# Optimization experiments

Measured on AMD Instinct MI355X. Metric: run time of the kernel, lower is better.

The kernel has to match this reference:

```python
import jax, jax.numpy as jnp
import numpy as np


def _conv(x, w, b=None, stride=1, pad=0, groups=1):
    y = jax.lax.conv_general_dilated(x, w, (stride, stride), [(pad, pad), (pad, pad)],
                                     feature_group_count=groups,
                                     dimension_numbers=('NCHW', 'OIHW', 'NCHW'))
    return y if b is None else y + b[None, :, None, None]


def _ln_c(x, g, b, eps=1e-5):
    # LayerNorm2d: normalize over channel axis of NCHW
    mu = x.mean(axis=1, keepdims=True)
    var = ((x - mu) ** 2).mean(axis=1, keepdims=True)
    return (x - mu) * jax.lax.rsqrt(var + eps) * g[None, :, None, None] + b[None, :, None, None]


def _ln_last(x, g, b, eps=1e-5):
    mu = x.mean(-1, keepdims=True)
    var = ((x - mu) ** 2).mean(-1, keepdims=True)
    return (x - mu) * jax.lax.rsqrt(var + eps) * g + b


def _resize(x, hw):
    B, C, _, _ = x.shape
    return jax.image.resize(x, (B, C, hw[0], hw[1]), method='bilinear')


def _ss2d(x, in_w, cv_w, cv_b, xp_w, dtp_w, dtp_b, Alog, Dsk, on_g, on_b, out_w):
    # x: (B,H,W,C) channels-last; VMamba SS2D v2 (cross-scan selective scan)
    B, H, W, C = x.shape
    D = in_w.shape[0] // 2
    K, Ck, _ = xp_w.shape
    R = dtp_w.shape[-1]
    N = (Ck - R) // 2
    L = H * W
    xz = x @ in_w.T                                   # (B,H,W,2D)
    xc, z = jnp.split(xz, 2, axis=-1)
    xc = jax.nn.silu(_conv(jnp.transpose(xc, (0, 3, 1, 2)), cv_w, cv_b, pad=1, groups=D))
    x0 = xc.reshape(B, D, L)
    x1 = jnp.transpose(xc, (0, 1, 3, 2)).reshape(B, D, L)
    xs = jnp.stack([x0, x1, jnp.flip(x0, -1), jnp.flip(x1, -1)], axis=1)  # (B,K,D,L)
    x_dbl = jnp.einsum('bkdl,kcd->bkcl', xs, xp_w)
    dts, Bs, Cs = jnp.split(x_dbl, [R, R + N], axis=2)
    dt = jax.nn.softplus(jnp.einsum('bkrl,kdr->bkdl', dts, dtp_w) + dtp_b[None, :, :, None])
    A = -jnp.exp(Alog).reshape(K, D, N)
    a = jnp.exp(dt[..., None] * A[None, :, :, None, :])                  # (B,K,D,L,N)
    bmat = (dt * xs)[..., None] * jnp.transpose(Bs, (0, 1, 3, 2))[:, :, None, :, :]

    def comb(e1, e2):
        a1, b1 = e1
        a2, b2 = e2
        return a1 * a2, a2 * b1 + b2

    _, h = jax.lax.associative_scan(comb, (a, bmat), axis=3)             # h: (B,K,D,L,N)
    y = jnp.einsum('bkdln,bknl->bkdl', h, Cs) + Dsk.reshape(K, D)[None, :, :, None] * xs

    def inv_t(t):
        return jnp.transpose(t.reshape(B, D, W, H), (0, 1, 3, 2)).reshape(B, D, L)

    ym = y[:, 0] + inv_t(y[:, 1]) + jnp.flip(y[:, 2], -1) + inv_t(jnp.flip(y[:, 3], -1))
    ym = _ln_last(jnp.transpose(ym.reshape(B, D, H, W), (0, 2, 3, 1)), on_g, on_b)
    return (ym * jax.nn.silu(z)) @ out_w.T


def _mcfa(x, shortcut, q_w, q_b, sr_w, sr_b, srn_g, srn_b, k_w, k_b, v_w, v_b, mp_w, mp_b,
          key_dim=16, sr=2):
    # cross attention: queries from x, keys/values from spatially-reduced shortcut
    B, C, H, W = x.shape
    heads = C // key_dim
    q = _conv(x, q_w, q_b).reshape(B, heads, key_dim, H * W)
    s = _ln_c(_conv(shortcut, sr_w, sr_b, stride=sr), srn_g, srn_b)
    Lk = s.shape[2] * s.shape[3]
    k = _conv(s, k_w, k_b).reshape(B, heads, key_dim, Lk)
    v = _conv(s, v_w, v_b).reshape(B, heads, C // heads, Lk)
    scale = float(key_dim) ** 0.5
    attn = jax.nn.softmax(jnp.einsum('bhdq,bhdk->bhqk', q, k) / scale, axis=-1)
    o = jnp.einsum('bhqk,bhdk->bhdq', attn, v).reshape(B, C, H, W)
    return _conv(o, mp_w, mp_b)


def _forward(x, res, shortcut_mfkm, rc0_w, rcp_w, rcp_g, rcp_b, pe_w, pe_b,
             n1_g, n1_b, n2_g, n2_b, q_w, q_b, sr_w, sr_b, srn_g, srn_b,
             k_w, k_b, v_w, v_b, mp_w, mp_b, in_w, cv_w, cv_b, xp_w, dtp_w, dtp_b,
             Alog, Dsk, on_g, on_b, out_w, ls1_w, ls1_b, ls2_w, ls2_b,
             f1_w, f1_b, f2_w, f2_b):
    # Res_conv
    pad1 = res.mean(axis=1, keepdims=True)
    pad2 = res.max(axis=1, keepdims=True)
    r = jnp.concatenate([_conv(res, rc0_w), pad1, pad2], axis=1)          # (B,66,H,W)
    B, Ct, H, W = r.shape
    r = jnp.transpose(r.reshape(B, Ct // 3, 3, H, W), (0, 2, 1, 3, 4)).reshape(B, Ct, H, W)
    r = _conv(r, rcp_w, pad=1)
    bn_scale = rcp_g * jax.lax.rsqrt(jnp.float32(1.0 + 1e-5))             # eval BN, mean=0 var=1
    r = jnp.clip(r * bn_scale[None, :, None, None] + rcp_b[None, :, None, None], 0.0, 6.0)
    sm = _resize(shortcut_mfkm, (H, W))
    shortcut = jnp.concatenate([r, sm], axis=1)                           # 130 channels
    inp = _resize(x, (2 * x.shape[2], 2 * x.shape[3]))
    # _forward of the block (is_first=True, is_last=False, eval: dropout/droppath identity)
    t = inp + _conv(inp, pe_w, pe_b, pad=1, groups=inp.shape[1])
    m = _mcfa(_ln_c(t, n1_g, n1_b), shortcut, q_w, q_b, sr_w, sr_b, srn_g, srn_b,
              k_w, k_b, v_w, v_b, mp_w, mp_b)
    m = jnp.transpose(_ss2d(jnp.transpose(m, (0, 2, 3, 1)), in_w, cv_w, cv_b, xp_w,
                            dtp_w, dtp_b, Alog, Dsk, on_g, on_b, out_w), (0, 3, 1, 2))
    t = t * ls1_w[None, :, None, None] + ls1_b[None, :, None, None] + m   # layerscale_1 + residual
    u = _conv(_ln_c(t, n2_g, n2_b), f1_w, f1_b)
    u = _conv(jax.nn.gelu(u, approximate=False), f2_w, f2_b)
    t = t * ls2_w[None, :, None, None] + ls2_b[None, :, None, None] + u   # layerscale_2 + mlp
    return t


def setup_inputs():
    key = jax.random.key(0)
    ks = iter(jax.random.split(key, 64))

    def rn(shape, s=0.02):
        return jax.random.normal(next(ks), shape, dtype=jnp.float32) * s

    B, C, Hin, Win, RC, CD, Ct, Din, K, N, R, MH = 2, 64, 32, 32, 32, 130, 66, 128, 4, 16, 4, 256
    return {
        'x': rn((B, C, Hin, Win), 1.0),
        'res': rn((B, RC, 2 * Hin, 2 * Win), 1.0),
        'shortcut_mfkm': rn((B, C, Hin, Win), 1.0),
        'rc0_w': rn((C, RC, 1, 1)),
        'rcp_w': rn((Ct, Ct, 3, 3)),
        'rcp_g': jnp.ones((Ct,), jnp.float32),
        'rcp_b': jnp.zeros((Ct,), jnp.float32),
        'pe_w': rn((C, 1, 3, 3)),
        'pe_b': jnp.zeros((C,), jnp.float32),
        'n1_g': jnp.ones((C,), jnp.float32),
        'n1_b': jnp.zeros((C,), jnp.float32),
        'n2_g': jnp.ones((C,), jnp.float32),
        'n2_b': jnp.zeros((C,), jnp.float32),
        'q_w': rn((C, C, 1, 1)),
        'q_b': jnp.zeros((C,), jnp.float32),
        'sr_w': rn((CD, CD, 2, 2)),
        'sr_b': jnp.zeros((CD,), jnp.float32),
        'srn_g': jnp.ones((CD,), jnp.float32),
        'srn_b': jnp.zeros((CD,), jnp.float32),
        'k_w': rn((C, CD, 1, 1)),
        'k_b': jnp.zeros((C,), jnp.float32),
        'v_w': rn((C, CD, 1, 1)),
        'v_b': jnp.zeros((C,), jnp.float32),
        'mp_w': rn((C, C, 1, 1)),
        'mp_b': jnp.zeros((C,), jnp.float32),
        'in_w': rn((2 * Din, C)),
        'cv_w': rn((Din, 1, 3, 3)),
        'cv_b': jnp.zeros((Din,), jnp.float32),
        'xp_w': rn((K, R + 2 * N, Din)),
        'dtp_w': rn((K, Din, R), 0.1),
        'dtp_b': rn((K, Din), 0.1),
        'Alog': jnp.log(jnp.tile(jnp.arange(1, N + 1, dtype=jnp.float32), (K * Din, 1))),
        'Dsk': jnp.ones((K * Din,), jnp.float32),
        'on_g': jnp.ones((Din,), jnp.float32),
        'on_b': jnp.zeros((Din,), jnp.float32),
        'out_w': rn((C, Din)),
        'ls1_w': jnp.full((C,), 1e-5, jnp.float32),
        'ls1_b': jnp.zeros((C,), jnp.float32),
        'ls2_w': jnp.full((C,), 1e-5, jnp.float32),
        'ls2_b': jnp.zeros((C,), jnp.float32),
        'f1_w': rn((MH, C, 1, 1)),
        'f1_b': jnp.zeros((MH,), jnp.float32),
        'f2_w': rn((C, MH, 1, 1)),
        'f2_b': jnp.zeros((C,), jnp.float32),
    }


def reference(x, res, shortcut_mfkm, rc0_w, rcp_w, rcp_g, rcp_b, pe_w, pe_b,
              n1_g, n1_b, n2_g, n2_b, q_w, q_b, sr_w, sr_b, srn_g, srn_b,
              k_w, k_b, v_w, v_b, mp_w, mp_b, in_w, cv_w, cv_b, xp_w, dtp_w, dtp_b,
              Alog, Dsk, on_g, on_b, out_w, ls1_w, ls1_b, ls2_w, ls2_b,
              f1_w, f1_b, f2_w, f2_b):
    t = _forward(x, res, shortcut_mfkm, rc0_w, rcp_w, rcp_g, rcp_b, pe_w, pe_b,
                 n1_g, n1_b, n2_g, n2_b, q_w, q_b, sr_w, sr_b, srn_g, srn_b,
                 k_w, k_b, v_w, v_b, mp_w, mp_b, in_w, cv_w, cv_b, xp_w, dtp_w, dtp_b,
                 Alog, Dsk, on_g, on_b, out_w, ls1_w, ls1_b, ls2_w, ls2_b,
                 f1_w, f1_b, f2_w, f2_b)
    return (t, t)  # (x, shortcut) with shortcut == x in the non-last branch
```

## Files before the change

### kernel.cpp

```cpp
#include <hip/hip_runtime.h>
#include <math.h>

#define B2 2
#define HW 4096
#define L4 4096
#define NCH 16
#define CLEN 256

enum : size_t {
  OFF_INP    = 0,
  OFF_SHORT  = 524288,
  OFF_RSHUF  = 1589248,
  OFF_XLN    = 2129920,
  OFF_SRAW   = 2654208,
  OFF_SRED   = 2920448,
  OFF_QT     = 3186688,
  OFF_KT     = 3710976,
  OFF_VT     = 3842048,
  OFF_OT     = 3973120,
  OFF_M0     = 4497408,
  OFF_XC     = 3186688,
  OFF_U1     = 0,
  OFF_T      = 5021696,
  OFF_T1     = 5545984,
  OFF_Z      = 6070272,
  OFF_XC2    = 7118848,
  OFF_XC2T   = 8167424,
  OFF_PROJ   = 9216000,
  OFF_APROD  = 10395648,
  OFF_HEND   = 10657792,
  OFF_SSTART = 10919936,
  OFF_YM     = 11182080,
  OFF_PART   = 7118848,
};

__global__ void k_rconv0(const float* __restrict__ res, const float* __restrict__ rc0_w,
                         float* __restrict__ rshuf) {
  int idx = blockIdx.x * 256 + threadIdx.x;
  if (idx >= B2 * 66 * HW) return;
  int p = idx & (HW - 1);
  int bc = idx >> 12;
  int c = bc % 66, b = bc / 66;
  int cc = (c % 22) * 3 + (c / 22);
  const float* rb = res + (size_t)b * 32 * HW + p;
  float v;
  if (cc < 64) {
    const float* w = rc0_w + cc * 32;
    float a = 0.f;
#pragma unroll
    for (int ic = 0; ic < 32; ++ic) a = fmaf(w[ic], rb[ic * HW], a);
    v = a;
  } else if (cc == 64) {
    float s = 0.f;
#pragma unroll
    for (int ic = 0; ic < 32; ++ic) s += rb[ic * HW];
    v = s * (1.f / 32.f);
  } else {
    float m = rb[0];
#pragma unroll
    for (int ic = 1; ic < 32; ++ic) m = fmaxf(m, rb[ic * HW]);
    v = m;
  }
  rshuf[idx] = v;
}

__global__ __launch_bounds__(256) void k_rconv3(const float* __restrict__ rshuf,
                                                const float* __restrict__ rcp_w,
                                                const float* __restrict__ rcp_g,
                                                const float* __restrict__ rcp_b,
                                                float* __restrict__ shortcut) {
  __shared__ float lw[6 * 594];
  int cg = blockIdx.y % 11, b = blockIdx.y / 11;
  int c0 = cg * 6;
  for (int i = threadIdx.x; i < 6 * 594; i += 256) lw[i] = rcp_w[c0 * 594 + i];
  __syncthreads();
  int p = blockIdx.x * 256 + threadIdx.x;
  int h = p >> 6, w = p & 63;
  float acc[6] = {0, 0, 0, 0, 0, 0};
  for (int ci = 0; ci < 66; ++ci) {
    const float* ib = rshuf + (size_t)(b * 66 + ci) * HW;
#pragma unroll
    for (int kh = -1; kh <= 1; ++kh) {
      int hh = h + kh;
      if (hh < 0 || hh > 63) continue;
#pragma unroll
      for (int kw = -1; kw <= 1; ++kw) {
        int ww = w + kw;
        if (ww < 0 || ww > 63) continue;
        float x = ib[hh * 64 + ww];
        int tap = ci * 9 + (kh + 1) * 3 + (kw + 1);
#pragma unroll
        for (int u = 0; u < 6; ++u) acc[u] = fmaf(lw[u * 594 + tap], x, acc[u]);
      }
    }
  }
  const float bscale = rsqrtf(1.f + 1e-5f);
#pragma unroll
  for (int u = 0; u < 6; ++u) {
    int co = c0 + u;
    float v = acc[u] * (rcp_g[co] * bscale) + rcp_b[co];
    v = fminf(fmaxf(v, 0.f), 6.f);
    shortcut[(size_t)(b * 130 + co) * HW + p] = v;
  }
}

__global__ void k_up(const float* __restrict__ smf, const float* __restrict__ x,
                     float* __restrict__ shortcut, float* __restrict__ inp) {
  int idx = blockIdx.x * 256 + threadIdx.x;
  if (idx >= B2 * 128 * HW) return;
  int p = idx & (HW - 1);
  int bc = idx >> 12;
  int c = bc & 127, b = bc >> 7;
  int oh = p >> 6, ow = p & 63;
  int hp = oh >> 1, wp = ow >> 1;
  int ih0, ih1, iw0, iw1;
  float wh0, ww0;
  if (oh & 1) { ih0 = hp; ih1 = (hp + 1 > 31) ? 31 : hp + 1; wh0 = 0.75f; }
  else        { ih0 = (hp - 1 < 0) ? 0 : hp - 1; ih1 = hp; wh0 = 0.25f; }
  if (ow & 1) { iw0 = wp; iw1 = (wp + 1 > 31) ? 31 : wp + 1; ww0 = 0.75f; }
  else        { iw0 = (wp - 1 < 0) ? 0 : wp - 1; iw1 = wp; ww0 = 0.25f; }
  const float* src = (c < 64) ? (smf + (size_t)(b * 64 + c) * 1024)
                              : (x + (size_t)(b * 64 + (c - 64)) * 1024);
  float v00 = src[ih0 * 32 + iw0], v01 = src[ih0 * 32 + iw1];
  float v10 = src[ih1 * 32 + iw0], v11 = src[ih1 * 32 + iw1];
  float v = wh0 * (ww0 * v00 + (1.f - ww0) * v01) + (1.f - wh0) * (ww0 * v10 + (1.f - ww0) * v11);
  if (c < 64) shortcut[(size_t)(b * 130 + 66 + c) * HW + p] = v;
  else        inp[(size_t)(b * 64 + (c - 64)) * HW + p] = v;
}

__global__ void k_pe(const float* __restrict__ inp, const float* __restrict__ pe_w,
                     const float* __restrict__ pe_b, float* __restrict__ t) {
  int idx = blockIdx.x * 256 + threadIdx.x;
  if (idx >= B2 * 64 * HW) return;
  int p = idx & (HW - 1);
  int bc = idx >> 12;
  int c = bc & 63;
  int h = p >> 6, w = p & 63;
  const float* ib = inp + (size_t)bc * HW;
  const float* wt = pe_w + c * 9;
  float a = pe_b[c];
#pragma unroll
  for (int kh = -1; kh <= 1; ++kh) {
    int hh = h + kh;
    if (hh < 0 || hh > 63) continue;
#pragma unroll
    for (int kw = -1; kw <= 1; ++kw) {
      int ww = w + kw;
      if (ww < 0 || ww > 63) continue;
      a = fmaf(wt[(kh + 1) * 3 + (kw + 1)], ib[hh * 64 + ww], a);
    }
  }
  t[idx] = ib[p] + a;
}

__global__ void k_lnc64(const float* __restrict__ in, const float* __restrict__ g,
                        const float* __restrict__ bb, float* __restrict__ out) {
  int idx = blockIdx.x * 256 + threadIdx.x;
  if (idx >= B2 * HW) return;
  int p = idx & (HW - 1), b = idx >> 12;
  const float* ib = in + (size_t)b * 64 * HW + p;
  float s = 0.f, sq = 0.f;
#pragma unroll 8
  for (int c = 0; c < 64; ++c) { float v = ib[c * HW]; s += v; sq = fmaf(v, v, sq); }
  float mu = s * (1.f / 64.f);
  float var = sq * (1.f / 64.f) - mu * mu;
  float rs = rsqrtf(var + 1e-5f);
  float* ob = out + (size_t)b * 64 * HW + p;
#pragma unroll 8
  for (int c = 0; c < 64; ++c) ob[c * HW] = (ib[c * HW] - mu) * rs * g[c] + bb[c];
}

__global__ __launch_bounds__(256) void k_sr(const float* __restrict__ shortcut,
                                            const float* __restrict__ sr_w,
                                            const float* __restrict__ sr_b,
                                            float* __restrict__ sraw) {
  __shared__ float lw[5 * 520];
  int cg = blockIdx.y % 26, b = blockIdx.y / 26;
  int c0 = cg * 5;
  for (int i = threadIdx.x; i < 5 * 520; i += 256) lw[i] = sr_w[c0 * 520 + i];
  __syncthreads();
  int op = blockIdx.x * 256 + threadIdx.x;
  int oh = op >> 5, ow = op & 31;
  const float* ib = shortcut + (size_t)b * 130 * HW + (oh * 2) * 64 + ow * 2;
  float acc[5] = {0, 0, 0, 0, 0};
  for (int ci = 0; ci < 130; ++ci) {
    const float* q = ib + (size_t)ci * HW;
    float x00 = q[0], x01 = q[1], x10 = q[64], x11 = q[65];
#pragma unroll
    for (int u = 0; u < 5; ++u) {
      const float* wp = lw + u * 520 + ci * 4;
      acc[u] = fmaf(wp[0], x00, fmaf(wp[1], x01, fmaf(wp[2], x10, fmaf(wp[3], x11, acc[u]))));
    }
  }
#pragma unroll
  for (int u = 0; u < 5; ++u)
    sraw[(size_t)(b * 130 + c0 + u) * 1024 + op] = acc[u] + sr_b[c0 + u];
}

__global__ __launch_bounds__(64) void k_ln130(const float* __restrict__ sraw,
                                              const float* __restrict__ g,
                                              const float* __restrict__ bb,
                                              float* __restrict__ sred) {
  int op = blockIdx.x & 1023, b = blockIdx.x >> 10;
  int t = threadIdx.x;
  const float* ib = sraw + (size_t)b * 130 * 1024 + op;
  float s = 0.f, sq = 0.f;
  for (int c = t; c < 130; c += 64) { float v = ib[c * 1024]; s += v; sq = fmaf(v, v, sq); }
#pragma unroll
  for (int off = 32; off; off >>= 1) { s += __shfl_xor(s, off); sq += __shfl_xor(sq, off); }
  float mu = s * (1.f / 130.f);
  float var = sq * (1.f / 130.f) - mu * mu;
  float rs = rsqrtf(var + 1e-5f);
  float* ob = sred + (size_t)b * 130 * 1024 + op;
  for (int c = t; c < 130; c += 64) ob[c * 1024] = (ib[c * 1024] - mu) * rs * g[c] + bb[c];
}

__global__ void k_kv(const float* __restrict__ sred, const float* __restrict__ k_w,
                     const float* __restrict__ k_b, const float* __restrict__ v_w,
                     const float* __restrict__ v_b, float* __restrict__ kt, float* __restrict__ vt) {
  int idx = blockIdx.x * 256 + threadIdx.x;
  if (idx >= B2 * 128 * 1024) return;
  int op = idx & 1023;
  int bc = idx >> 10;
  int c = bc & 127, b = bc >> 7;
  bool isv = c >= 64;
  int co = c & 63;
  const float* w = (isv ? v_w : k_w) + co * 130;
  const float* ib = sred + (size_t)b * 130 * 1024 + op;
  float a = (isv ? v_b : k_b)[co];
  for (int ci = 0; ci < 130; ++ci) a = fmaf(w[ci], ib[ci * 1024], a);
  float* dst = isv ? vt : kt;
  dst[((size_t)(b * 4 + (co >> 4)) * 1024 + op) * 16 + (co & 15)] = a;
}

__global__ void k_q(const float* __restrict__ xln, const float* __restrict__ q_w,
                    const float* __restrict__ q_b, float* __restrict__ qt) {
  int idx = blockIdx.x * 256 + threadIdx.x;
  if (idx >= B2 * 64 * HW) return;
  int p = idx & (HW - 1);
  int bc = idx >> 12;
  int co = bc & 63, b = bc >> 6;
  const float* ib = xln + (size_t)b * 64 * HW + p;
  const float* w = q_w + co * 64;
  float a = q_b[co];
#pragma unroll
  for (int ci = 0; ci < 64; ++ci) a = fmaf(w[ci], ib[ci * HW], a);
  qt[((size_t)(b * 4 + (co >> 4)) * HW + p) * 16 + (co & 15)] = a;
}

__global__ __launch_bounds__(256) void k_attn1(const float* __restrict__ qt,
                                               const float* __restrict__ kt,
                                               const float* __restrict__ vt,
                                               float* __restrict__ part) {
  __shared__ float sk[256 * 16];
  __shared__ float sv[256 * 16];
  int ktile = blockIdx.x, qtile = blockIdx.y, bh = blockIdx.z;
  int tid = threadIdx.x;
  const float* kb = kt + ((size_t)bh * 1024 + ktile * 256) * 16;
  const float* vb = vt + ((size_t)bh * 1024 + ktile * 256) * 16;
  for (int i = tid * 4; i < 4096; i += 1024) {
    *(float4*)&sk[i] = *(const float4*)&kb[i];
    *(float4*)&sv[i] = *(const float4*)&vb[i];
  }
  __syncthreads();
  int q = qtile * 256 + tid;
  const float4* qr = (const float4*)(qt + ((size_t)bh * HW + q) * 16);
  float4 q0 = qr[0], q1 = qr[1], q2 = qr[2], q3 = qr[3];
  const float sc = 0.25f;
  q0.x *= sc; q0.y *= sc; q0.z *= sc; q0.w *= sc;
  q1.x *= sc; q1.y *= sc; q1.z *= sc; q1.w *= sc;
  q2.x *= sc; q2.y *= sc; q2.z *= sc; q2.w *= sc;
  q3.x *= sc; q3.y *= sc; q3.z *= sc; q3.w *= sc;
  float m = -1e30f, l = 0.f;
  float acc[16];
#pragma unroll
  for (int i = 0; i < 16; ++i) acc[i] = 0.f;
  for (int kk = 0; kk < 256; ++kk) {
    const float4* kr = (const float4*)&sk[kk * 16];
    float4 a0 = kr[0], a1 = kr[1], a2 = kr[2], a3 = kr[3];
    float s = q0.x * a0.x + q0.y * a0.y + q0.z * a0.z + q0.w * a0.w
            + q1.x * a1.x + q1.y * a1.y + q1.z * a1.z + q1.w * a1.w
            + q2.x * a2.x + q2.y * a2.y + q2.z * a2.z + q2.w * a2.w
            + q3.x * a3.x + q3.y * a3.y + q3.z * a3.z + q3.w * a3.w;
    if (s > m) {
      float r = __expf(m - s);
      l *= r;
#pragma unroll
      for (int i = 0; i < 16; ++i) acc[i] *= r;
      m = s;
    }
    float pe = __expf(s - m);
    l += pe;
    const float4* vr = (const float4*)&sv[kk * 16];
    float4 b0 = vr[0], b1 = vr[1], b2 = vr[2], b3 = vr[3];
    acc[0] = fmaf(pe, b0.x, acc[0]);  acc[1] = fmaf(pe, b0.y, acc[1]);
    acc[2] = fmaf(pe, b0.z, acc[2]);  acc[3] = fmaf(pe, b0.w, acc[3]);
    acc[4] = fmaf(pe, b1.x, acc[4]);  acc[5] = fmaf(pe, b1.y, acc[5]);
    acc[6] = fmaf(pe, b1.z, acc[6]);  acc[7] = fmaf(pe, b1.w, acc[7]);
    acc[8] = fmaf(pe, b2.x, acc[8]);  acc[9] = fmaf(pe, b2.y, acc[9]);
    acc[10] = fmaf(pe, b2.z, acc[10]); acc[11] = fmaf(pe, b2.w, acc[11]);
    acc[12] = fmaf(pe, b3.x, acc[12]); acc[13] = fmaf(pe, b3.y, acc[13]);
    acc[14] = fmaf(pe, b3.z, acc[14]); acc[15] = fmaf(pe, b3.w, acc[15]);
  }
  float* o = part + (((size_t)bh * 4 + ktile) * HW + q) * 18;
#pragma unroll
  for (int i = 0; i < 16; ++i) o[i] = acc[i];
  o[16] = m;
  o[17] = l;
}

__global__ void k_attn2(const float* __restrict__ part, float* __restrict__ ot) {
  int idx = blockIdx.x * 256 + threadIdx.x;
  if (idx >= B2 * 4 * HW) return;
  int q = idx & (HW - 1), bh = idx >> 12;
  float M = -1e30f;
#pragma unroll
  for (int kt4 = 0; kt4 < 4; ++kt4)
    M = fmaxf(M, part[(((size_t)bh * 4 + kt4) * HW + q) * 18 + 16]);
  float L = 0.f;
  float o[16];
#pragma unroll
  for (int i = 0; i < 16; ++i) o[i] = 0.f;
#pragma unroll
  for (int kt4 = 0; kt4 < 4; ++kt4) {
    const float* p = part + (((size_t)bh * 4 + kt4) * HW + q) * 18;
    float w = __expf(p[16] - M);
    L = fmaf(p[17], w, L);
#pragma unroll
    for (int i = 0; i < 16; ++i) o[i] = fmaf(p[i], w, o[i]);
  }
  float inv = 1.f / L;
  float* ob = ot + ((size_t)bh * HW + q) * 16;
#pragma unroll
  for (int i = 0; i < 16; ++i) ob[i] = o[i] * inv;
}

__global__ void k_mp(const float* __restrict__ ot, const float* __restrict__ mp_w,
                     const float* __restrict__ mp_b, float* __restrict__ m0) {
  int idx = blockIdx.x * 256 + threadIdx.x;
  if (idx >= B2 * 64 * HW) return;
  int p = idx & (HW - 1);
  int bc = idx >> 12;
  int co = bc & 63, b = bc >> 6;
  const float* w = mp_w + co * 64;
  float a = mp_b[co];
#pragma unroll
  for (int h = 0; h < 4; ++h) {
    const float* ob = ot + ((size_t)(b * 4 + h) * HW + p) * 16;
#pragma unroll
    for (int d = 0; d < 16; ++d) a = fmaf(w[h * 16 + d], ob[d], a);
  }
  m0[idx] = a;
}

__global__ __launch_bounds__(256) void k_inproj(const float* __restrict__ m0,
                                                const float* __restrict__ in_w,
                                                float* __restrict__ xc, float* __restrict__ z) {
  __shared__ float lw[4 * 64];
  int jg = blockIdx.y & 63, b = blockIdx.y >> 6;
  int j0 = jg * 4;
  for (int i = threadIdx.x; i < 256; i += 256) lw[i] = in_w[j0 * 64 + i];
  __syncthreads();
  int p = blockIdx.x * 256 + threadIdx.x;
  const float* ib = m0 + (size_t)b * 64 * HW + p;
  float acc[4] = {0, 0, 0, 0};
#pragma unroll 8
  for (int ci = 0; ci < 64; ++ci) {
    float x = ib[ci * HW];
#pragma unroll
    for (int u = 0; u < 4; ++u) acc[u] = fmaf(lw[u * 64 + ci], x, acc[u]);
  }
#pragma unroll
  for (int u = 0; u < 4; ++u) {
    int j = j0 + u;
    if (j < 128) xc[(size_t)(b * 128 + j) * HW + p] = acc[u];
    else         z[(size_t)(b * 128 + j - 128) * HW + p] = acc[u];
  }
}

__global__ void k_dw(const float* __restrict__ xc, const float* __restrict__ cv_w,
                     const float* __restrict__ cv_b, float* __restrict__ xc2) {
  int idx = blockIdx.x * 256 + threadIdx.x;
  if (idx >= B2 * 128 * HW) return;
  int p = idx & (HW - 1);
  int bc = idx >> 12;
  int c = bc & 127;
  int h = p >> 6, w = p & 63;
  const float* ib = xc + (size_t)bc * HW;
  const float* wt = cv_w + c * 9;
  float a = cv_b[c];
#pragma unroll
  for (int kh = -1; kh <= 1; ++kh) {
    int hh = h + kh;
    if (hh < 0 || hh > 63) continue;
#pragma unroll
    for (int kw = -1; kw <= 1; ++kw) {
      int ww = w + kw;
      if (ww < 0 || ww > 63) continue;
      a = fmaf(wt[(kh + 1) * 3 + (kw + 1)], ib[hh * 64 + ww], a);
    }
  }
  xc2[idx] = a / (1.f + __expf(-a));
}

__global__ void k_tr(const float* __restrict__ xc2, float* __restrict__ xc2t) {
  int idx = blockIdx.x * 256 + threadIdx.x;
  if (idx >= B2 * 128 * HW) return;
  int l = idx & (HW - 1);
  size_t bd = (size_t)(idx >> 12);
  xc2t[idx] = xc2[(bd << 12) + ((l & 63) << 6) + (l >> 6)];
}

__global__ __launch_bounds__(256) void k_projs(const float* __restrict__ xc2,
                                               const float* __restrict__ xc2t,
                                               const float* __restrict__ xp_w,
                                               float* __restrict__ proj) {
  __shared__ float lw[6 * 128];
  int cg = blockIdx.y % 6;
  int bk = blockIdx.y / 6;
  int b = bk >> 2, k = bk & 3;
  int c0 = cg * 6;
  for (int i = threadIdx.x; i < 768; i += 256) lw[i] = xp_w[(k * 36 + c0) * 128 + i];
  __syncthreads();
  int l = blockIdx.x * 256 + threadIdx.x;
  const float* src = ((k & 1) ? xc2t : xc2) + (size_t)b * 128 * HW;
  int lx = (k >= 2) ? (4095 - l) : l;
  float acc[6] = {0, 0, 0, 0, 0, 0};
#pragma unroll 4
  for (int d = 0; d < 128; ++d) {
    float x = src[(size_t)d * HW + lx];
#pragma unroll
    for (int u = 0; u < 6; ++u) acc[u] = fmaf(lw[u * 128 + d], x, acc[u]);
  }
#pragma unroll
  for (int u = 0; u < 6; ++u)
    proj[(size_t)(bk * 36 + c0 + u) * L4 + l] = acc[u];
}

template <int PC>
__global__ __launch_bounds__(256) void k_scan(const float* __restrict__ proj,
                                              const float* __restrict__ xc2,
                                              const float* __restrict__ xc2t,
                                              const float* __restrict__ dtp_w,
                                              const float* __restrict__ dtp_b,
                                              const float* __restrict__ Alog,
                                              const float* __restrict__ Dsk,
                                              float* __restrict__ aprod,
                                              float* __restrict__ hend,
                                              const float* __restrict__ sstart,
                                              float* __restrict__ ympre) {
  int ch = blockIdx.x, dg = blockIdx.y, bk = blockIdx.z;
  int b = bk >> 2, k = bk & 3;
  int tid = threadIdx.x;
  int n = tid & 15, dl = tid >> 4;
  int d = dg * 16 + dl;
  int kd = k * 128 + d;
  float Ad = -__expf(Alog[kd * 16 + n]);
  const float* wr = dtp_w + kd * 4;
  float w0 = wr[0], w1 = wr[1], w2 = wr[2], w3 = wr[3];
  float db = dtp_b[kd];
  const float* pb = proj + (size_t)bk * 36 * L4;
  const float* srcb = ((k & 1) ? xc2t : xc2) + (size_t)b * 128 * HW;
  bool rev = (k >= 2);
  float h = PC ? sstart[((size_t)(bk * 128 + d) * 16 + n) * NCH + ch] : 0.f;
  float ap = 1.f;
  float Dv = PC ? Dsk[kd] : 0.f;
  __shared__ float sdts[4][16];
  __shared__ float sB[16][17];
  __shared__ float sC[16][17];
  __shared__ float sx[16][16];
  __shared__ float sdt[16][16];
  int l0 = ch * CLEN;
  for (int t0 = 0; t0 < CLEN; t0 += 16) {
    int lb = l0 + t0;
    __syncthreads();
    if (tid < 64) sdts[tid >> 4][tid & 15] = pb[(size_t)(tid >> 4) * L4 + lb + (tid & 15)];
    sB[dl][n] = pb[(size_t)(4 + dl) * L4 + lb + n];
    if (PC) sC[dl][n] = pb[(size_t)(20 + dl) * L4 + lb + n];
    {
      int l = lb + n;
      int lx = rev ? (4095 - l) : l;
      sx[dl][n] = srcb[(size_t)(dg * 16 + dl) * HW + lx];
    }
    __syncthreads();
    {
      float xr = fmaf(w0, sdts[0][n], fmaf(w1, sdts[1][n], fmaf(w2, sdts[2][n], fmaf(w3, sdts[3][n], db))));
      float spv = (xr > 20.f) ? xr : log1pf(__expf(xr));
      sdt[dl][n] = spv;
    }
    __syncthreads();
#pragma unroll 4
    for (int t = 0; t < 16; ++t) {
      float dt = sdt[dl][t];
      float xs = sx[dl][t];
      float a = __expf(dt * Ad);
      h = fmaf(a, h, dt * xs * sB[n][t]);
      if (PC) {
        float yv = h * sC[n][t];
        yv += __shfl_xor(yv, 1);
        yv += __shfl_xor(yv, 2);
        yv += __shfl_xor(yv, 4);
        yv += __shfl_xor(yv, 8);
        if (n == 0) {
          int l = lb + t;
          int pp;
          if (k == 0) pp = l;
          else if (k == 1) pp = ((l & 63) << 6) | (l >> 6);
          else if (k == 2) pp = 4095 - l;
          else { int lf = 4095 - l; pp = ((lf & 63) << 6) | (lf >> 6); }
          atomicAdd(ympre + ((size_t)b * HW + pp) * 128 + d, yv + Dv * xs);
        }
      } else {
        ap *= a;
      }
    }
  }
  if (!PC) {
    size_t o = ((size_t)(bk * 128 + d) * 16 + n) * NCH + ch;
    aprod[o] = ap;
    hend[o] = h;
  }
}

__global__ void k_scanB(const float* __restrict__ aprod, const float* __restrict__ hend,
                        float* __restrict__ sstart) {
  int idx = blockIdx.x * 256 + threadIdx.x;
  if (idx >= B2 * 4 * 128 * 16) return;
  const float* ap = aprod + (size_t)idx * NCH;
  const float* he = hend + (size_t)idx * NCH;
  float* ss = sstart + (size_t)idx * NCH;
  float s = 0.f;
#pragma unroll
  for (int c = 0; c < NCH; ++c) { ss[c] = s; s = fmaf(ap[c], s, he[c]); }
}

__global__ __launch_bounds__(128) void k_merge(const float* __restrict__ ympre,
                                               const float* __restrict__ z,
                                               const float* __restrict__ on_g,
                                               const float* __restrict__ on_b,
                                               float* __restrict__ g) {
  int p = blockIdx.x & (HW - 1), b = blockIdx.x >> 12;
  int d = threadIdx.x;
  float v = ympre[((size_t)b * HW + p) * 128 + d];
  float s = v, sq = v * v;
#pragma unroll
  for (int off = 32; off; off >>= 1) { s += __shfl_xor(s, off); sq += __shfl_xor(sq, off); }
  __shared__ float sh[4];
  if ((threadIdx.x & 63) == 0) { sh[(threadIdx.x >> 6) * 2] = s; sh[(threadIdx.x >> 6) * 2 + 1] = sq; }
  __syncthreads();
  float S = sh[0] + sh[2], SQ = sh[1] + sh[3];
  float mu = S * (1.f / 128.f);
  float var = SQ * (1.f / 128.f) - mu * mu;
  float rs = rsqrtf(var + 1e-5f);
  float gn = (v - mu) * rs * on_g[d] + on_b[d];
  float zv = z[((size_t)(b * 128 + d)) * HW + p];
  float sil = zv / (1.f + __expf(-zv));
  g[((size_t)b * HW + p) * 128 + d] = gn * sil;
}

__global__ __launch_bounds__(256) void k_outproj(const float* __restrict__ g,
                                                 const float* __restrict__ out_w,
                                                 const float* __restrict__ t,
                                                 const float* __restrict__ ls1_w,
                                                 const float* __restrict__ ls1_b,
                                                 float* __restrict__ t1) {
  __shared__ float lw[4 * 128];
  int cg = blockIdx.y & 15, b = blockIdx.y >> 4;
  int c0 = cg * 4;
  for (int i = threadIdx.x; i < 512; i += 256) lw[i] = out_w[c0 * 128 + i];
  __syncthreads();
  int p = blockIdx.x * 256 + threadIdx.x;
  const float* gr = g + ((size_t)b * HW + p) * 128;
  float acc[4] = {0, 0, 0, 0};
#pragma unroll 4
  for (int dd = 0; dd < 128; ++dd) {
    float x = gr[dd];
#pragma unroll
    for (int u = 0; u < 4; ++u) acc[u] = fmaf(lw[u * 128 + dd], x, acc[u]);
  }
#pragma unroll
  for (int u = 0; u < 4; ++u) {
    int co = c0 + u;
    size_t o = (size_t)(b * 64 + co) * HW + p;
    t1[o] = fmaf(t[o], ls1_w[co], ls1_b[co]) + acc[u];
  }
}

__global__ __launch_bounds__(256) void k_f1(const float* __restrict__ xln2,
                                            const float* __restrict__ f1_w,
                                            const float* __restrict__ f1_b,
                                            float* __restrict__ u1) {
  __shared__ float lw[8 * 64];
  int cg = blockIdx.y & 31, b = blockIdx.y >> 5;
  int c0 = cg * 8;
  for (int i = threadIdx.x; i < 512; i += 256) lw[i] = f1_w[c0 * 64 + i];
  __syncthreads();
  int p = blockIdx.x * 256 + threadIdx.x;
  const float* ib = xln2 + (size_t)b * 64 * HW + p;
  float acc[8] = {0, 0, 0, 0, 0, 0, 0, 0};
#pragma unroll 8
  for (int ci = 0; ci < 64; ++ci) {
    float x = ib[ci * HW];
#pragma unroll
    for (int u = 0; u < 8; ++u) acc[u] = fmaf(lw[u * 64 + ci], x, acc[u]);
  }
#pragma unroll
  for (int u = 0; u < 8; ++u) {
    float v = acc[u] + f1_b[c0 + u];
    v = 0.5f * v * (1.f + erff(v * 0.70710678118654752440f));
    u1[(size_t)(b * 256 + c0 + u) * HW + p] = v;
  }
}

__global__ __launch_bounds__(256) void k_f2(const float* __restrict__ u1,
                                            const float* __restrict__ f2_w,
                                            const float* __restrict__ f2_b,
                                            const float* __restrict__ t1,
                                            const float* __restrict__ ls2_w,
                                            const float* __restrict__ ls2_b,
                                            float* __restrict__ out) {
  __shared__ float lw[4 * 256];
  int cg = blockIdx.y & 15, b = blockIdx.y >> 4;
  int c0 = cg * 4;
  for (int i = threadIdx.x; i < 1024; i += 256) lw[i] = f2_w[c0 * 256 + i];
  __syncthreads();
  int p = blockIdx.x * 256 + threadIdx.x;
  const float* ib = u1 + (size_t)b * 256 * HW + p;
  float acc[4] = {0, 0, 0, 0};
#pragma unroll 4
  for (int ci = 0; ci < 256; ++ci) {
    float x = ib[(size_t)ci * HW];
#pragma unroll
    for (int u = 0; u < 4; ++u) acc[u] = fmaf(lw[u * 256 + ci], x, acc[u]);
  }
#pragma unroll
  for (int u = 0; u < 4; ++u) {
    int co = c0 + u;
    size_t o = (size_t)(b * 64 + co) * HW + p;
    float v = fmaf(t1[o], ls2_w[co], ls2_b[co]) + acc[u] + f2_b[co];
    out[o] = v;
    out[o + (size_t)B2 * 64 * HW] = v;
  }
}

extern "C" void kernel_launch(void* const* d_in, const int* in_sizes, int n_in,
                              void* d_out, int out_size, void* d_ws, size_t ws_size,
                              hipStream_t stream) {
  const float* x     = (const float*)d_in[0];
  const float* res   = (const float*)d_in[1];
  const float* smf   = (const float*)d_in[2];
  const float* rc0_w = (const float*)d_in[3];
  const float* rcp_w = (const float*)d_in[4];
  const float* rcp_g = (const float*)d_in[5];
  const float* rcp_b = (const float*)d_in[6];
  const float* pe_w  = (const float*)d_in[7];
  const float* pe_b  = (const float*)d_in[8];
  const float* n1_g  = (const float*)d_in[9];
  const float* n1_b  = (const float*)d_in[10];
  const float* n2_g  = (const float*)d_in[11];
  const float* n2_b  = (const float*)d_in[12];
  const float* q_w   = (const float*)d_in[13];
  const float* q_b   = (const float*)d_in[14];
  const float* sr_w  = (const float*)d_in[15];
  const float* sr_b  = (const float*)d_in[16];
  const float* srn_g = (const float*)d_in[17];
  const float* srn_b = (const float*)d_in[18];
  const float* k_w   = (const float*)d_in[19];
  const float* k_b   = (const float*)d_in[20];
  const float* v_w   = (const float*)d_in[21];
  const float* v_b   = (const float*)d_in[22];
  const float* mp_w  = (const float*)d_in[23];
  const float* mp_b  = (const float*)d_in[24];
  const float* in_w  = (const float*)d_in[25];
  const float* cv_w  = (const float*)d_in[26];
  const float* cv_b  = (const float*)d_in[27];
  const float* xp_w  = (const float*)d_in[28];
  const float* dtp_w = (const float*)d_in[29];
  const float* dtp_b = (const float*)d_in[30];
  const float* Alog  = (const float*)d_in[31];
  const float* Dsk   = (const float*)d_in[32];
  const float* on_g  = (const float*)d_in[33];
  const float* on_b  = (const float*)d_in[34];
  const float* out_w = (const float*)d_in[35];
  const float* ls1_w = (const float*)d_in[36];
  const float* ls1_b = (const float*)d_in[37];
  const float* ls2_w = (const float*)d_in[38];
  const float* ls2_b = (const float*)d_in[39];
  const float* f1_w  = (const float*)d_in[40];
  const float* f1_b  = (const float*)d_in[41];
  const float* f2_w  = (const float*)d_in[42];
  const float* f2_b  = (const float*)d_in[43];
  float* ws = (float*)d_ws;
  float* out = (float*)d_out;

  k_rconv0<<<dim3(2112), dim3(256), 0, stream>>>(res, rc0_w, ws + OFF_RSHUF);
  k_rconv3<<<dim3(16, 22), dim3(256), 0, stream>>>(ws + OFF_RSHUF, rcp_w, rcp_g, rcp_b, ws + OFF_SHORT);
  k_up<<<dim3(4096), dim3(256), 0, stream>>>(smf, x, ws + OFF_SHORT, ws + OFF_INP);
  k_pe<<<dim3(2048), dim3(256), 0, stream>>>(ws + OFF_INP, pe_w, pe_b, ws + OFF_T);
  k_lnc64<<<dim3(32), dim3(256), 0, stream>>>(ws + OFF_T, n1_g, n1_b, ws + OFF_XLN);
  k_sr<<<dim3(4, 52), dim3(256), 0, stream>>>(ws + OFF_SHORT, sr_w, sr_b, ws + OFF_SRAW);
  k_ln130<<<dim3(2048), dim3(64), 0, stream>>>(ws + OFF_SRAW, srn_g, srn_b, ws + OFF_SRED);
  k_kv<<<dim3(1024), dim3(256), 0, stream>>>(ws + OFF_SRED, k_w, k_b, v_w, v_b, ws + OFF_KT, ws + OFF_VT);
  k_q<<<dim3(2048), dim3(256), 0, stream>>>(ws + OFF_XLN, q_w, q_b, ws + OFF_QT);
  k_attn1<<<dim3(4, 16, 8), dim3(256), 0, stream>>>(ws + OFF_QT, ws + OFF_KT, ws + OFF_VT, ws + OFF_PART);
  k_attn2<<<dim3(128), dim3(256), 0, stream>>>(ws + OFF_PART, ws + OFF_OT);
  k_mp<<<dim3(2048), dim3(256), 0, stream>>>(ws + OFF_OT, mp_w, mp_b, ws + OFF_M0);
  k_inproj<<<dim3(16, 128), dim3(256), 0, stream>>>(ws + OFF_M0, in_w, ws + OFF_XC, ws + OFF_Z);
  k_dw<<<dim3(4096), dim3(256), 0, stream>>>(ws + OFF_XC, cv_w, cv_b, ws + OFF_XC2);
  k_tr<<<dim3(4096), dim3(256), 0, stream>>>(ws + OFF_XC2, ws + OFF_XC2T);
  k_projs<<<dim3(16, 48), dim3(256), 0, stream>>>(ws + OFF_XC2, ws + OFF_XC2T, xp_w, ws + OFF_PROJ);
  k_scan<0><<<dim3(NCH, 8, 8), dim3(256), 0, stream>>>(ws + OFF_PROJ, ws + OFF_XC2, ws + OFF_XC2T,
      dtp_w, dtp_b, Alog, Dsk, ws + OFF_APROD, ws + OFF_HEND, ws + OFF_SSTART, ws + OFF_YM);
  k_scanB<<<dim3(64), dim3(256), 0, stream>>>(ws + OFF_APROD, ws + OFF_HEND, ws + OFF_SSTART);
  hipMemsetAsync(ws + OFF_YM, 0, (size_t)B2 * HW * 128 * sizeof(float), stream);
  k_scan<1><<<dim3(NCH, 8, 8), dim3(256), 0, stream>>>(ws + OFF_PROJ, ws + OFF_XC2, ws + OFF_XC2T,
      dtp_w, dtp_b, Alog, Dsk, ws + OFF_APROD, ws + OFF_HEND, ws + OFF_SSTART, ws + OFF_YM);
  k_merge<<<dim3(8192), dim3(128), 0, stream>>>(ws + OFF_YM, ws + OFF_Z, on_g, on_b, ws + OFF_YM);
  k_outproj<<<dim3(16, 32), dim3(256), 0, stream>>>(ws + OFF_YM, out_w, ws + OFF_T, ls1_w, ls1_b, ws + OFF_T1);
  k_lnc64<<<dim3(32), dim3(256), 0, stream>>>(ws + OFF_T1, n2_g, n2_b, ws + OFF_XLN);
  k_f1<<<dim3(16, 64), dim3(256), 0, stream>>>(ws + OFF_XLN, f1_w, f1_b, ws + OFF_U1);
  k_f2<<<dim3(16, 32), dim3(256), 0, stream>>>(ws + OFF_U1, f2_w, f2_b, ws + OFF_T1, ls2_w, ls2_b, out);
}
```

Before: 621.0 us.

## Restructure selective scan: one thread per channel holding all 16 states, 64 chunks

The chunked selective scan now gives each thread one channel d and keeps all 16 state entries in registers, instead of one thread per (d,n) with shuffle reductions. The sequence is split into 64 chunks of 64 rather than 16 of 256. The chunk decay product is computed as exp(A*sum(dt)) instead of a running product, and chunk state buffers move to a chunk-major layout in reused workspace. This aims to remove per-step warp shuffles, to load dt/B/C/x once per block, and to shorten the serial path per chunk, at the cost of more registers and a longer cross-chunk pass in scanB.

```diff
diff --git a/kernel.cpp b/kernel.cpp
--- a/kernel.cpp
+++ b/kernel.cpp
@@ -4,10 +4,12 @@
 #define B2 2
 #define HW 4096
 #define L4 4096
-#define NCH 16
-#define CLEN 256
+#define NCH 64
 
 enum : size_t {
+  OFF_APROD  = 0,
+  OFF_HEND   = 1048576,
+  OFF_SSTART = 2097152,
   OFF_INP    = 0,
   OFF_SHORT  = 524288,
   OFF_RSHUF  = 1589248,
@@ -27,9 +29,6 @@
   OFF_XC2    = 7118848,
   OFF_XC2T   = 8167424,
   OFF_PROJ   = 9216000,
-  OFF_APROD  = 10395648,
-  OFF_HEND   = 10657792,
-  OFF_SSTART = 10919936,
   OFF_YM     = 11182080,
   OFF_PART   = 7118848,
 };
@@ -438,100 +437,147 @@
 }
 
 template <int PC>
-__global__ __launch_bounds__(256) void k_scan(const float* __restrict__ proj,
-                                              const float* __restrict__ xc2,
-                                              const float* __restrict__ xc2t,
-                                              const float* __restrict__ dtp_w,
-                                              const float* __restrict__ dtp_b,
-                                              const float* __restrict__ Alog,
-                                              const float* __restrict__ Dsk,
-                                              float* __restrict__ aprod,
-                                              float* __restrict__ hend,
-                                              const float* __restrict__ sstart,
-                                              float* __restrict__ ympre) {
-  int ch = blockIdx.x, dg = blockIdx.y, bk = blockIdx.z;
+__global__ __launch_bounds__(256) void k_scan2(const float* __restrict__ proj,
+                                               const float* __restrict__ xc2,
+                                               const float* __restrict__ xc2t,
+                                               const float* __restrict__ dtp_w,
+                                               const float* __restrict__ dtp_b,
+                                               const float* __restrict__ Alog,
+                                               const float* __restrict__ Dsk,
+                                               float* __restrict__ aprod,
+                                               float* __restrict__ hend,
+                                               const float* __restrict__ sstart,
+                                               float* __restrict__ ympre) {
+  __shared__ float sxs[2][128][33];
+  __shared__ float sB[2][16][32];
+  __shared__ float sC[2][16][32];
+  __shared__ float sdts[2][4][32];
+  int tid = threadIdx.x;
+  int hid = tid >> 7;
+  int dl = tid & 127;
+  int ch = blockIdx.x * 2 + hid;
+  int bk = blockIdx.y;
   int b = bk >> 2, k = bk & 3;
-  int tid = threadIdx.x;
-  int n = tid & 15, dl = tid >> 4;
-  int d = dg * 16 + dl;
+  int d = dl;
   int kd = k * 128 + d;
-  float Ad = -__expf(Alog[kd * 16 + n]);
-  const float* wr = dtp_w + kd * 4;
-  float w0 = wr[0], w1 = wr[1], w2 = wr[2], w3 = wr[3];
+  float Ad[16];
+  {
+    const float4* a4 = (const float4*)(Alog + (size_t)kd * 16);
+#pragma unroll
+    for (int i = 0; i < 4; ++i) {
+      float4 v = a4[i];
+      Ad[i * 4 + 0] = -__expf(v.x); Ad[i * 4 + 1] = -__expf(v.y);
+      Ad[i * 4 + 2] = -__expf(v.z); Ad[i * 4 + 3] = -__expf(v.w);
+    }
+  }
+  float4 wv = *(const float4*)(dtp_w + (size_t)kd * 4);
   float db = dtp_b[kd];
+  float Dv = PC ? Dsk[kd] : 0.f;
+  float h[16];
+  if (PC) {
+    const float4* s4 = (const float4*)(sstart + (size_t)ch * 16384 + (size_t)(bk * 128 + d) * 16);
+#pragma unroll
+    for (int i = 0; i < 4; ++i) {
+      float4 v = s4[i];
+      h[i * 4 + 0] = v.x; h[i * 4 + 1] = v.y; h[i * 4 + 2] = v.z; h[i * 4 + 3] = v.w;
+    }
+  } else {
+#pragma unroll
+    for (int i = 0; i < 16; ++i) h[i] = 0.f;
+  }
+  float ssum = 0.f;
   const float* pb = proj + (size_t)bk * 36 * L4;
   const float* srcb = ((k & 1) ? xc2t : xc2) + (size_t)b * 128 * HW;
   bool rev = (k >= 2);
-  float h = PC ? sstart[((size_t)(bk * 128 + d) * 16 + n) * NCH + ch] : 0.f;
-  float ap = 1.f;
-  float Dv = PC ? Dsk[kd] : 0.f;
-  __shared__ float sdts[4][16];
-  __shared__ float sB[16][17];
-  __shared__ float sC[16][17];
-  __shared__ float sx[16][16];
-  __shared__ float sdt[16][16];
-  int l0 = ch * CLEN;
-  for (int t0 = 0; t0 < CLEN; t0 += 16) {
-    int lb = l0 + t0;
+
+  for (int tile = 0; tile < 2; ++tile) {
+    int lb = ch * 64 + tile * 32;
     __syncthreads();
-    if (tid < 64) sdts[tid >> 4][tid & 15] = pb[(size_t)(tid >> 4) * L4 + lb + (tid & 15)];
-    sB[dl][n] = pb[(size_t)(4 + dl) * L4 + lb + n];
-    if (PC) sC[dl][n] = pb[(size_t)(20 + dl) * L4 + lb + n];
-    {
-      int l = lb + n;
+#pragma unroll
+    for (int i = 0; i < 9; ++i) {
+      int flat = i * 128 + dl;
+      int row = flat >> 5, col = flat & 31;
+      float v = pb[(size_t)row * L4 + lb + col];
+      if (row < 4) sdts[hid][row][col] = v;
+      else if (row < 20) sB[hid][row - 4][col] = v;
+      else sC[hid][row - 20][col] = v;
+    }
+#pragma unroll
+    for (int i = 0; i < 32; ++i) {
+      int flat = i * 128 + dl;
+      int dd = flat >> 5, t = flat & 31;
+      int l = lb + t;
       int lx = rev ? (4095 - l) : l;
-      sx[dl][n] = srcb[(size_t)(dg * 16 + dl) * HW + lx];
+      sxs[hid][dd][t] = srcb[(size_t)dd * HW + lx];
     }
     __syncthreads();
-    {
-      float xr = fmaf(w0, sdts[0][n], fmaf(w1, sdts[1][n], fmaf(w2, sdts[2][n], fmaf(w3, sdts[3][n], db))));
-      float spv = (xr > 20.f) ? xr : log1pf(__expf(xr));
-      sdt[dl][n] = spv;
-    }
-    __syncthreads();
-#pragma unroll 4
-    for (int t = 0; t < 16; ++t) {
-      float dt = sdt[dl][t];
-      float xs = sx[dl][t];
-      float a = __expf(dt * Ad);
-      h = fmaf(a, h, dt * xs * sB[n][t]);
+#pragma unroll
+    for (int tg = 0; tg < 32; tg += 4) {
+      float spv[4], xsv[4], dxs[4];
+#pragma unroll
+      for (int j = 0; j < 4; ++j) {
+        int t = tg + j;
+        float dtr = fmaf(wv.x, sdts[hid][0][t], fmaf(wv.y, sdts[hid][1][t],
+                    fmaf(wv.z, sdts[hid][2][t], fmaf(wv.w, sdts[hid][3][t], db))));
+        float sp = (dtr > 20.f) ? dtr : log1pf(__expf(dtr));
+        spv[j] = sp;
+        xsv[j] = sxs[hid][dl][t];
+        dxs[j] = sp * xsv[j];
+        if (!PC) ssum += sp;
+      }
+      float y[4] = {0.f, 0.f, 0.f, 0.f};
+#pragma unroll
+      for (int n = 0; n < 16; ++n) {
+        float hv = h[n], adn = Ad[n];
+        float4 B4 = *(const float4*)&sB[hid][n][tg];
+        if (PC) {
+          float4 C4 = *(const float4*)&sC[hid][n][tg];
+          hv = fmaf(__expf(spv[0] * adn), hv, dxs[0] * B4.x); y[0] = fmaf(hv, C4.x, y[0]);
+          hv = fmaf(__expf(spv[1] * adn), hv, dxs[1] * B4.y); y[1] = fmaf(hv, C4.y, y[1]);
+          hv = fmaf(__expf(spv[2] * adn), hv, dxs[2] * B4.z); y[2] = fmaf(hv, C4.z, y[2]);
+          hv = fmaf(__expf(spv[3] * adn), hv, dxs[3] * B4.w); y[3] = fmaf(hv, C4.w, y[3]);
+        } else {
+          hv = fmaf(__expf(spv[0] * adn), hv, dxs[0] * B4.x);
+          hv = fmaf(__expf(spv[1] * adn), hv, dxs[1] * B4.y);
+          hv = fmaf(__expf(spv[2] * adn), hv, dxs[2] * B4.z);
+          hv = fmaf(__expf(spv[3] * adn), hv, dxs[3] * B4.w);
+        }
+        h[n] = hv;
+      }
       if (PC) {
-        float yv = h * sC[n][t];
-        yv += __shfl_xor(yv, 1);
-        yv += __shfl_xor(yv, 2);
-        yv += __shfl_xor(yv, 4);
-        yv += __shfl_xor(yv, 8);
-        if (n == 0) {
-          int l = lb + t;
+#pragma unroll
+        for (int j = 0; j < 4; ++j) {
+          int l = lb + tg + j;
           int pp;
           if (k == 0) pp = l;
           else if (k == 1) pp = ((l & 63) << 6) | (l >> 6);
           else if (k == 2) pp = 4095 - l;
           else { int lf = 4095 - l; pp = ((lf & 63) << 6) | (lf >> 6); }
-          atomicAdd(ympre + ((size_t)b * HW + pp) * 128 + d, yv + Dv * xs);
+          atomicAdd(ympre + ((size_t)b * HW + pp) * 128 + d, y[j] + Dv * xsv[j]);
         }
-      } else {
-        ap *= a;
       }
     }
   }
   if (!PC) {
-    size_t o = ((size_t)(bk * 128 + d) * 16 + n) * NCH + ch;
-    aprod[o] = ap;
-    hend[o] = h;
+    size_t base = (size_t)ch * 16384 + (size_t)(bk * 128 + d) * 16;
+#pragma unroll
+    for (int i = 0; i < 16; ++i) {
+      aprod[base + i] = __expf(Ad[i] * ssum);
+      hend[base + i] = h[i];
+    }
   }
 }
 
 __global__ void k_scanB(const float* __restrict__ aprod, const float* __restrict__ hend,
                         float* __restrict__ sstart) {
   int idx = blockIdx.x * 256 + threadIdx.x;
-  if (idx >= B2 * 4 * 128 * 16) return;
-  const float* ap = aprod + (size_t)idx * NCH;
-  const float* he = hend + (size_t)idx * NCH;
-  float* ss = sstart + (size_t)idx * NCH;
+  if (idx >= 16384) return;
   float s = 0.f;
-#pragma unroll
-  for (int c = 0; c < NCH; ++c) { ss[c] = s; s = fmaf(ap[c], s, he[c]); }
+  for (int c = 0; c < NCH; ++c) {
+    size_t o = (size_t)c * 16384 + idx;
+    sstart[o] = s;
+    s = fmaf(aprod[o], s, hend[o]);
+  }
 }
 
 __global__ __launch_bounds__(128) void k_merge(const float* __restrict__ ympre,
@@ -709,11 +755,11 @@
   k_dw<<<dim3(4096), dim3(256), 0, stream>>>(ws + OFF_XC, cv_w, cv_b, ws + OFF_XC2);
   k_tr<<<dim3(4096), dim3(256), 0, stream>>>(ws + OFF_XC2, ws + OFF_XC2T);
   k_projs<<<dim3(16, 48), dim3(256), 0, stream>>>(ws + OFF_XC2, ws + OFF_XC2T, xp_w, ws + OFF_PROJ);
-  k_scan<0><<<dim3(NCH, 8, 8), dim3(256), 0, stream>>>(ws + OFF_PROJ, ws + OFF_XC2, ws + OFF_XC2T,
+  k_scan2<0><<<dim3(NCH / 2, 8), dim3(256), 0, stream>>>(ws + OFF_PROJ, ws + OFF_XC2, ws + OFF_XC2T,
       dtp_w, dtp_b, Alog, Dsk, ws + OFF_APROD, ws + OFF_HEND, ws + OFF_SSTART, ws + OFF_YM);
   k_scanB<<<dim3(64), dim3(256), 0, stream>>>(ws + OFF_APROD, ws + OFF_HEND, ws + OFF_SSTART);
   hipMemsetAsync(ws + OFF_YM, 0, (size_t)B2 * HW * 128 * sizeof(float), stream);
-  k_scan<1><<<dim3(NCH, 8, 8), dim3(256), 0, stream>>>(ws + OFF_PROJ, ws + OFF_XC2, ws + OFF_XC2T,
+  k_scan2<1><<<dim3(NCH / 2, 8), dim3(256), 0, stream>>>(ws + OFF_PROJ, ws + OFF_XC2, ws + OFF_XC2T,
       dtp_w, dtp_b, Alog, Dsk, ws + OFF_APROD, ws + OFF_HEND, ws + OFF_SSTART, ws + OFF_YM);
   k_merge<<<dim3(8192), dim3(128), 0, stream>>>(ws + OFF_YM, ws + OFF_Z, on_g, on_b, ws + OFF_YM);
   k_outproj<<<dim3(16, 32), dim3(256), 0, stream>>>(ws + OFF_YM, out_w, ws + OFF_T, ls1_w, ls1_b, ws + OFF_T1);
```

New measurement: 636.0 us. +2.4%, slower.
